# Performance work log

Measured on AMD Instinct MI355X. Metric: run time of the kernel, lower is better.

Reference implementation:

```python
import jax, jax.numpy as jnp
import numpy as np

NEG = -9999.0      # chart init / clip floor (np.clip a_min=-9999.0)
THRESH = -9000.0   # 'pseudo_score > -9000' acceptance gate
ARC_BONUS = 5.0    # '+ 5' added to every arc candidate


def _fill_chart(vinfo):
    """Eisner DP chart fill, faithful to the sequential numpy triple loop.
    vinfo: [N, N] arc scores. Returns (score_chart [N,N,2,2], backtrace [N,N,2,2]).
    Chart axes: [i, j, direction, completeness] as in the torch source.
    Parallelized over span start i and split q; sequential over width k via scan.
    Sequential-update subtleties of the original q-loop are reproduced exactly:
      * complete (0,1) at q=i reads the (0,0) cell as it stands after only the
        q=i incomplete update ('part00');
      * complete (1,1) at q=j reads the fully updated (1,0) cell ('new10');
      * complete (0,1) at q=j and (1,1) at q=i are strict-improvement no-ops;
      * ties keep the earliest q (jnp.argmax returns first occurrence).
    """
    N = vinfo.shape[0]
    idx = jnp.arange(N)
    ii = idx[:, None]   # span start i
    mm = idx[None, :]   # split offset m; q = i + m
    S = jnp.full((N, N, 2, 2), NEG, dtype=vinfo.dtype).at[idx, idx].set(0.0)
    BT = jnp.zeros((N, N, 2, 2), dtype=jnp.int32)

    def step(carry, k):
        S, BT = carry
        j = idx + k
        row_ok = j < N
        okb = row_ok[:, None]
        jc = jnp.minimum(j, N - 1)
        jb = jc[:, None]
        q = ii + mm
        qc = jnp.minimum(q, N - 1)
        q1c = jnp.minimum(q + 1, N - 1)

        # ---- incomplete spans (0,0) and (1,0): q in [i, j-1]  <=>  m in [0, k-1]
        base = jnp.where((mm < k) & okb,
                         S[:, :, 1, 1][ii, qc] + S[:, :, 0, 1][q1c, jb],
                         -jnp.inf)                      # [N (i), N (m)]
        vL = vinfo[jc, idx][:, None]   # vinfo[j, i] -> arc j<-...: head j
        vR = vinfo[idx, jc][:, None]   # vinfo[i, j]
        p00 = jnp.maximum(base + vL + ARC_BONUS, NEG)
        p10 = jnp.maximum(base + vR + ARC_BONUS, NEG)
        m00 = jnp.max(p00, axis=1); q00 = idx + jnp.argmax(p00, axis=1)
        m10 = jnp.max(p10, axis=1); q10 = idx + jnp.argmax(p10, axis=1)
        ok00 = row_ok & (m00 > THRESH)
        ok10 = row_ok & (m10 > THRESH)
        # chart[i,j,0,0] as it stands right after the q=i iteration
        part00 = jnp.where(row_ok & (p00[:, 0] > THRESH), p00[:, 0], NEG)
        new10 = jnp.where(ok10, m10, NEG)

        m_mid = (mm >= 1) & (mm < k) & okb
        # ---- complete (0,1): q=i uses partially built (0,0); q=j is a no-op
        c01 = jnp.where(m_mid, S[:, :, 0, 1][ii, qc] + S[:, :, 0, 0][qc, jb], -jnp.inf)
        c01 = c01.at[:, 0].set(jnp.where(row_ok, part00, -jnp.inf))
        p01 = jnp.maximum(c01, NEG)
        m01 = jnp.max(p01, axis=1); q01 = idx + jnp.argmax(p01, axis=1)
        ok01 = row_ok & (m01 > THRESH)

        # ---- complete (1,1): q=i is a no-op; q=j uses freshly updated (1,0)
        c11 = jnp.where(m_mid, S[:, :, 1, 0][ii, qc] + S[:, :, 1, 1][qc, jb], -jnp.inf)
        c11 = jnp.where((mm == k) & okb, new10[:, None], c11)
        p11 = jnp.maximum(c11, NEG)
        m11 = jnp.max(p11, axis=1); q11 = idx + jnp.argmax(p11, axis=1)
        ok11 = row_ok & (m11 > THRESH)

        def upd(S, BT, a, b, ok, val, qarg):
            S = S.at[idx, jc, a, b].set(jnp.where(ok, val, S[idx, jc, a, b]))
            BT = BT.at[idx, jc, a, b].set(
                jnp.where(ok, qarg, BT[idx, jc, a, b]).astype(jnp.int32))
            return S, BT

        S, BT = upd(S, BT, 0, 0, ok00, m00, q00)
        S, BT = upd(S, BT, 1, 0, ok10, m10, q10)
        S, BT = upd(S, BT, 0, 1, ok01, m01, q01)
        S, BT = upd(S, BT, 1, 1, ok11, m11, q11)
        return (S, BT), None

    (S, BT), _ = jax.lax.scan(step, (S, BT), jnp.arange(1, N))
    return S, BT


def setup_inputs() -> dict:
    key = jax.random.key(0)
    B, N = 64, 128
    b_vinfo_mtx = jax.random.normal(key, (B, N, N), dtype=jnp.float32)
    b_buffer_size = jnp.full((B,), N, dtype=jnp.int32)
    return {"b_vinfo_mtx": b_vinfo_mtx, "b_buffer_size": b_buffer_size}


def reference(b_vinfo_mtx, b_buffer_size):
    # All sentences use the full buffer (b_buffer_size == N), so the batch is
    # processed as one vmapped chart fill.
    scores, backtrace = jax.vmap(_fill_chart)(b_vinfo_mtx)
    return scores, backtrace
```

## Files before the change

### kernel.cpp

```cpp
#include <hip/hip_runtime.h>
#include <stdint.h>

static constexpr int kN = 128;
static constexpr int kTri = (kN * (kN - 1)) / 2;
static constexpr int kTriD = (kN * (kN + 1)) / 2;
static constexpr int kThreads = 1024;
static constexpr float kNeg = -9999.0f;
static constexpr float kThresh = -9000.0f;
static constexpr float kArcBonus = 5.0f;
static constexpr int kDynLds = kTriD * 16;
static constexpr int kCMax = 9;

__device__ __forceinline__ int rowBase(int i) { return (i * (2 * kN - 1 - i)) / 2; }
__device__ __forceinline__ int colBaseD(int c) { return (c * (c + 1)) / 2; }

__device__ __forceinline__ void ldsBarrier() {
    asm volatile("s_waitcnt lgkmcnt(0)\n\ts_barrier" ::: "memory");
}

template <int CTRL>
__device__ __forceinline__ float dppMax(float x) {
    const int y = __builtin_amdgcn_update_dpp(__float_as_int(x), __float_as_int(x),
                                              CTRL, 0xF, 0xF, true);
    return fmaxf(x, __int_as_float(y));
}
template <int CTRL>
__device__ __forceinline__ int dppMinI(int x) {
    const int y = __builtin_amdgcn_update_dpp(x, x, CTRL, 0xF, 0xF, true);
    return (y < x) ? y : x;
}

__device__ __forceinline__ int lpOf(int k) {
    if (k <= 16) return 0;
    if (k < 64) return 3;
    return 4;
}
__device__ __forceinline__ void mapStatic(int nk, int tid, int& i, int& j, bool& act) {
    const int lp = lpOf(nk);
    i = tid >> lp;
    j = i + nk;
    act = i < (kN - nk);
}

__device__ __forceinline__ float4 writeCell(float4* __restrict__ Q4,
                                            uint32_t* __restrict__ wsBT,
                                            int i, int j, int k,
                                            float gb, int ib, float vLc, float vRc,
                                            float v01, int i01, float v11, int i11) {
    const float v00 = (gb + vLc) + kArcBonus;
    const float v10 = (gb + vRc) + kArcBonus;
    const float new10 = (v10 > kThresh) ? v10 : kNeg;
    if (new10 > v11) { v11 = new10; i11 = k; }
    float4 w = make_float4(kNeg, kNeg, kNeg, kNeg);
    uint32_t p = 0;
    if (v00 > kThresh) { w.x = v00; p |= (uint32_t)(i + ib); }
    if (v01 > kThresh) { w.z = v01; p |= (uint32_t)(i + i01) << 8; }
    if (v10 > kThresh) { w.w = v10; p |= (uint32_t)(i + ib) << 16; }
    if (v11 > kThresh) { w.y = v11; p |= (uint32_t)(i + i11) << 24; }
    Q4[colBaseD(j) + i] = w;
    wsBT[rowBase(i) + k - 1] = p;
    return w;
}

__device__ __forceinline__ void doStepSerialReg(int k, int tid,
                                                float4* __restrict__ Q4,
                                                uint32_t* __restrict__ wsBT,
                                                const float* __restrict__ v,
                                                int& ci, int& cj, bool& cact,
                                                float& vL, float& vR,
                                                float (&sr11)[17], float (&sr01)[17],
                                                float (&sr10)[17]) {
    const int i = ci, j = cj;
    const bool act = cact;
    const float vLc = vL, vRc = vR;
    float bmax = -3.0e38f, v01 = -3.0e38f, v11 = -3.0e38f;
    int ib = 0, i01 = 0, i11 = 0x7FFFFFFF;
    if (act) {
        const int qjb = colBaseD(j);
        float4 cur = Q4[qjb + i + 1];
        bmax = cur.z; ib = 0;
        const float p00 = (cur.z + vLc) + kArcBonus;
        v01 = (p00 > kThresh) ? p00 : kNeg; i01 = 0;
#pragma unroll
        for (int m = 1; m < 16; ++m) {
            if (m < k) {
                const float4 nxt = Q4[qjb + i + m + 1];
                const float base = sr11[m] + nxt.z;
                const float p01v = sr01[m] + cur.x;
                const float p11v = sr10[m] + cur.y;
                if (base > bmax) { bmax = base; ib = m; }
                if (p01v > v01) { v01 = p01v; i01 = m; }
                if (p11v > v11) { v11 = p11v; i11 = m; }
                cur = nxt;
            }
        }
    }
    if (k + 1 < kN) {
        mapStatic(k + 1, tid, ci, cj, cact);
        vL = cact ? v[cj * kN + ci] : 0.f;
        vR = cact ? v[ci * kN + cj] : 0.f;
    }
    if (act) {
        const float4 w = writeCell(Q4, wsBT, i, j, k, bmax, ib, vLc, vRc,
                                   v01, i01, v11, i11);
        sr11[k] = w.y; sr01[k] = w.z; sr10[k] = w.w;
    }
}

template <int LP, int C>
__device__ __forceinline__ void preloadRow(int k0, int tid,
                                           const float4* __restrict__ Q4,
                                           float (&r11)[kCMax], float (&r01)[kCMax],
                                           float (&r10)[kCMax]) {
    constexpr int P = 1 << LP;
    const int i = tid >> LP;
    const int l = tid & (P - 1);
    const int mlo = l * C;
    const int mstart = mlo ? mlo : 1;
    const bool act = i < (kN - k0);
#pragma unroll
    for (int c = 0; c < C; ++c) {
        const int m = mstart + c;
        if (act && (m < mlo + C) && (m <= k0 - 1)) {
            const float4 d = Q4[colBaseD(i + m) + i];
            r11[c] = d.y; r01[c] = d.z; r10[c] = d.w;
        }
    }
}

template <int LP, int C>
__device__ __forceinline__ void fwInit(int k0, int tid,
                                       const float (&r11)[kCMax], const float (&r01)[kCMax],
                                       const float (&r10)[kCMax],
                                       float& fw11, float& fw01, float& fw10) {
    constexpr int P = 1 << LP;
    const int l = tid & (P - 1);
    const int mlo = l * C;
    const int mstart = mlo ? mlo : 1;
#pragma unroll
    for (int c = 0; c < C; ++c) {
        if (mstart + c == k0 - 1) { fw11 = r11[c]; fw01 = r01[c]; fw10 = r10[c]; }
    }
}

template <int LP, int C>
__device__ __forceinline__ void doStepC(int k, int tid,
                                        float4* __restrict__ Q4,
                                        uint32_t* __restrict__ wsBT,
                                        const float* __restrict__ v,
                                        int& ci, int& cj, bool& cact,
                                        float& vL, float& vR,
                                        float (&r11)[kCMax], float (&r01)[kCMax],
                                        float (&r10)[kCMax],
                                        float& fw11, float& fw01, float& fw10) {
    constexpr int P = 1 << LP;
    static_assert(P <= 16, "reductions must stay pure-DPP");
    const int i = ci, j = cj;
    const bool act = cact;
    const float vLc = vL, vRc = vR;
    const int l = tid & (P - 1);
    const int mlo = l * C;
    const int mstart = mlo ? mlo : 1;
    const int mhi = (mlo + C < k) ? (mlo + C) : k;
    const bool waveActive = (((tid & ~63) >> LP) < (kN - k));

    float bmax = -3.0e38f, v01 = -3.0e38f, v11 = -3.0e38f;
    int ib = 0x7FFFFFFF, i01 = 0x7FFFFFFF, i11 = 0x7FFFFFFF;

    const int mf = k - 1;
    const bool lact = waveActive && act && (mstart < mhi);
    const int qjb = colBaseD(j);
    float4 cur = make_float4(0.f, 0.f, 0.f, 0.f);
    if (lact) cur = Q4[qjb + i + mstart];
    if (act && mlo == 0) {
        bmax = cur.z; ib = 0;
        const float p00 = (cur.z + vLc) + kArcBonus;
        v01 = (p00 > kThresh) ? p00 : kNeg; i01 = 0;
    }
#pragma unroll
    for (int c = 0; c < C; ++c) {
        const int m = mstart + c;
        const bool isF = (m == mf);
        const float a11 = isF ? fw11 : r11[c];
        const float a01 = isF ? fw01 : r01[c];
        const float a10 = isF ? fw10 : r10[c];
        r11[c] = a11; r01[c] = a01; r10[c] = a10;
        const bool on = lact && (m < mhi);
        if (on) {
            const float4 nxt = Q4[qjb + i + m + 1];
            const float base = a11 + nxt.z;
            const float p01v = a01 + cur.x;
            const float p11v = a10 + cur.y;
            if (base > bmax) { bmax = base; ib = m; }
            if (p01v > v01) { v01 = p01v; i01 = m; }
            if (p11v > v11) { v11 = p11v; i11 = m; }
            cur = nxt;
        }
    }

    if (k + 1 < kN) {
        mapStatic(k + 1, tid, ci, cj, cact);
        vL = cact ? v[cj * kN + ci] : 0.f;
        vR = cact ? v[ci * kN + cj] : 0.f;
    }

    if (waveActive) {
        float gB = dppMax<0x141>(dppMax<0x4E>(dppMax<0xB1>(bmax)));
        float g01 = dppMax<0x141>(dppMax<0x4E>(dppMax<0xB1>(v01)));
        float g11 = dppMax<0x141>(dppMax<0x4E>(dppMax<0xB1>(v11)));
        if constexpr (P == 16) {
            gB = dppMax<0x140>(gB); g01 = dppMax<0x140>(g01); g11 = dppMax<0x140>(g11);
        }
        int cB = (bmax == gB) ? ib : 0x7FFFFFFF;
        int c01 = (v01 == g01) ? i01 : 0x7FFFFFFF;
        int c11 = (v11 == g11) ? i11 : 0x7FFFFFFF;
        cB = dppMinI<0x141>(dppMinI<0x4E>(dppMinI<0xB1>(cB)));
        c01 = dppMinI<0x141>(dppMinI<0x4E>(dppMinI<0xB1>(c01)));
        c11 = dppMinI<0x141>(dppMinI<0x4E>(dppMinI<0xB1>(c11)));
        if constexpr (P == 16) {
            cB = dppMinI<0x140>(cB); c01 = dppMinI<0x140>(c01); c11 = dppMinI<0x140>(c11);
        }

        const float v10f = (gB + vRc) + kArcBonus;
        const float new10 = (v10f > kThresh) ? v10f : kNeg;
        float v11m = g11;
        if (new10 > v11m) v11m = new10;
        fw11 = (v11m > kThresh) ? v11m : kNeg;
        fw01 = (g01 > kThresh) ? g01 : kNeg;
        fw10 = (v10f > kThresh) ? v10f : kNeg;

        if (act && l == 0) {
            writeCell(Q4, wsBT, i, j, k, gB, cB, vLc, vRc, g01, c01, g11, c11);
        }
    }
}

__global__ __launch_bounds__(kThreads) void eisner_dp(
    const float* __restrict__ vinfo,
    float* __restrict__ outS,
    float* __restrict__ outBT,
    uint32_t* __restrict__ btPacked)
{
    extern __shared__ float4 Q4[];

    const int tid = threadIdx.x;
    const int b = blockIdx.x;
    const float* v = vinfo + (size_t)b * kN * kN;
    uint32_t* wsBT = btPacked + (size_t)b * kTri;

    const float4 zeroq = make_float4(0.f, 0.f, 0.f, 0.f);
    if (tid < kN) Q4[colBaseD(tid) + tid] = zeroq;

    int ci, cj; bool cact;
    mapStatic(1, tid, ci, cj, cact);
    float vL = cact ? v[cj * kN + ci] : 0.f;
    float vR = cact ? v[ci * kN + cj] : 0.f;
    __syncthreads();

    {
        float sr11[17], sr01[17], sr10[17];
#pragma unroll
        for (int k = 1; k <= 16; ++k) {
            doStepSerialReg(k, tid, Q4, wsBT, v, ci, cj, cact, vL, vR,
                            sr11, sr01, sr10);
            ldsBarrier();
        }
    }

    float r11[kCMax], r01[kCMax], r10[kCMax];
    float fw11 = kNeg, fw01 = kNeg, fw10 = kNeg;
#pragma unroll
    for (int c = 0; c < kCMax; ++c) { r11[c] = kNeg; r01[c] = kNeg; r10[c] = kNeg; }

    preloadRow<3, 5>(17, tid, Q4, r11, r01, r10);
    fwInit<3, 5>(17, tid, r11, r01, r10, fw11, fw01, fw10);
    for (int k = 17; k < 40; ++k) {
        doStepC<3, 5>(k, tid, Q4, wsBT, v, ci, cj, cact, vL, vR,
                      r11, r01, r10, fw11, fw01, fw10);
        ldsBarrier();
    }
    preloadRow<3, 9>(40, tid, Q4, r11, r01, r10);
    fwInit<3, 9>(40, tid, r11, r01, r10, fw11, fw01, fw10);
    for (int k = 40; k < 64; ++k) {
        doStepC<3, 9>(k, tid, Q4, wsBT, v, ci, cj, cact, vL, vR,
                      r11, r01, r10, fw11, fw01, fw10);
        ldsBarrier();
    }
    preloadRow<4, 7>(64, tid, Q4, r11, r01, r10);
    fwInit<4, 7>(64, tid, r11, r01, r10, fw11, fw01, fw10);
    for (int k = 64; k < 112; ++k) {
        doStepC<4, 7>(k, tid, Q4, wsBT, v, ci, cj, cact, vL, vR,
                      r11, r01, r10, fw11, fw01, fw10);
        ldsBarrier();
    }
    preloadRow<4, 9>(112, tid, Q4, r11, r01, r10);
    fwInit<4, 9>(112, tid, r11, r01, r10, fw11, fw01, fw10);
    for (int k = 112; k < 128; ++k) {
        doStepC<4, 9>(k, tid, Q4, wsBT, v, ci, cj, cact, vL, vR,
                      r11, r01, r10, fw11, fw01, fw10);
        ldsBarrier();
    }

    __syncthreads();

    float4* gS4 = (float4*)(outS + (size_t)b * kN * kN * 4);
    float4* gB4 = (float4*)(outBT + (size_t)b * kN * kN * 4);
    const float4 negq = make_float4(kNeg, kNeg, kNeg, kNeg);
    for (int c = tid; c < kN * kN; c += kThreads) {
        const int i = c >> 7, j = c & (kN - 1);
        if (i < j) {
            const float4 q = Q4[colBaseD(j) + i];
            gS4[c] = make_float4(q.x, q.z, q.w, q.y);
            const uint32_t p = wsBT[rowBase(i) + (j - i - 1)];
            gB4[c] = make_float4((float)(p & 255u), (float)((p >> 8) & 255u),
                                 (float)((p >> 16) & 255u), (float)(p >> 24));
        } else if (i == j) {
            gS4[c] = zeroq;
            gB4[c] = zeroq;
        } else {
            gS4[c] = negq;
            gB4[c] = zeroq;
        }
    }
}

extern "C" void kernel_launch(void* const* d_in, const int* in_sizes, int n_in,
                              void* d_out, int out_size, void* d_ws, size_t ws_size,
                              hipStream_t stream) {
    (void)n_in; (void)out_size; (void)ws_size;
    const float* vinfo = (const float*)d_in[0];
    const int B = in_sizes[1];
    float* outS = (float*)d_out;
    float* outBT = outS + (size_t)B * kN * kN * 4;
    uint32_t* btPacked = (uint32_t*)d_ws;

    hipFuncSetAttribute(reinterpret_cast<const void*>(eisner_dp),
                        hipFuncAttributeMaxDynamicSharedMemorySize, kDynLds);

    eisner_dp<<<dim3(B), dim3(kThreads), kDynLds, stream>>>(vinfo, outS, outBT, btPacked);
}
```

Measured before the change: 236.4 us.

## Replace per-step block barriers with per-wave LDS flag point-to-point sync

Drops the workgroup-wide barrier after every DP width step. Each wave now spin-waits on an LDS flag published by its neighbouring wave, reflecting the one-sided dependency between span rows. Waves whose spans run out finish early and publish a sentinel, so the others are not held back by idle waves. The risks are spin-polling overhead, LDS memory-ordering issues with volatile flags, and deadlock if a dependency assumption is wrong.

```diff
diff --git a/kernel.cpp b/kernel.cpp
--- a/kernel.cpp
+++ b/kernel.cpp
@@ -8,15 +8,12 @@
 static constexpr float kNeg = -9999.0f;
 static constexpr float kThresh = -9000.0f;
 static constexpr float kArcBonus = 5.0f;
-static constexpr int kDynLds = kTriD * 16;
+static constexpr int kFlagInts = 5 * 17;
+static constexpr int kDynLds = kTriD * 16 + kFlagInts * 4;
 static constexpr int kCMax = 9;
 
 __device__ __forceinline__ int rowBase(int i) { return (i * (2 * kN - 1 - i)) / 2; }
 __device__ __forceinline__ int colBaseD(int c) { return (c * (c + 1)) / 2; }
-
-__device__ __forceinline__ void ldsBarrier() {
-    asm volatile("s_waitcnt lgkmcnt(0)\n\ts_barrier" ::: "memory");
-}
 
 template <int CTRL>
 __device__ __forceinline__ float dppMax(float x) {
@@ -28,6 +25,15 @@
 __device__ __forceinline__ int dppMinI(int x) {
     const int y = __builtin_amdgcn_update_dpp(x, x, CTRL, 0xF, 0xF, true);
     return (y < x) ? y : x;
+}
+
+__device__ __forceinline__ void spinWait(volatile const int* f, int need) {
+    while (*f < need) __builtin_amdgcn_s_sleep(2);
+    asm volatile("" ::: "memory");
+}
+__device__ __forceinline__ void publish(volatile int* f, int val, int laneId) {
+    asm volatile("s_waitcnt lgkmcnt(0)" ::: "memory");
+    if (laneId == 0) *f = val;
 }
 
 __device__ __forceinline__ int lpOf(int k) {
@@ -235,6 +241,48 @@
     }
 }
 
+__device__ __forceinline__ void runPhaseSerial(int tid, int laneId, int w,
+        float4* __restrict__ Q4, volatile int* flg,
+        uint32_t* __restrict__ wsBT, const float* __restrict__ v) {
+    if ((w << 6) >= kN - 1) return;
+    int ci, cj; bool cact;
+    mapStatic(1, tid, ci, cj, cact);
+    float vL = cact ? v[cj * kN + ci] : 0.f;
+    float vR = cact ? v[ci * kN + cj] : 0.f;
+    float sr11[17], sr01[17], sr10[17];
+#pragma unroll
+    for (int k = 1; k <= 16; ++k) {
+        spinWait(flg + (w + 1), k - 1);
+        doStepSerialReg(k, tid, Q4, wsBT, v, ci, cj, cact, vL, vR, sr11, sr01, sr10);
+        publish(flg + w, k, laneId);
+    }
+}
+
+template <int LP, int C>
+__device__ __forceinline__ void runPhaseC(int k0, int k1, int tid, int laneId, int w,
+        float4* __restrict__ Q4, volatile int* flg,
+        uint32_t* __restrict__ wsBT, const float* __restrict__ v,
+        float (&r11)[kCMax], float (&r01)[kCMax], float (&r10)[kCMax]) {
+    const int firstGroup = (w << 6) >> LP;
+    if (firstGroup >= kN - k0) return;
+    int ci, cj; bool cact;
+    mapStatic(k0, tid, ci, cj, cact);
+    float vL = cact ? v[cj * kN + ci] : 0.f;
+    float vR = cact ? v[ci * kN + cj] : 0.f;
+    float fw11 = kNeg, fw01 = kNeg, fw10 = kNeg;
+    preloadRow<LP, C>(k0, tid, Q4, r11, r01, r10);
+    fwInit<LP, C>(k0, tid, r11, r01, r10, fw11, fw01, fw10);
+    const int kD = kN - firstGroup;
+    const int kEnd = (k1 < kD) ? k1 : kD;
+    for (int k = k0; k < kEnd; ++k) {
+        spinWait(flg + (w + 1), k - 1);
+        doStepC<LP, C>(k, tid, Q4, wsBT, v, ci, cj, cact, vL, vR,
+                       r11, r01, r10, fw11, fw01, fw10);
+        publish(flg + w, k, laneId);
+    }
+    if (kD < k1) publish(flg + w, 127, laneId);
+}
+
 __global__ __launch_bounds__(kThreads) void eisner_dp(
     const float* __restrict__ vinfo,
     float* __restrict__ outS,
@@ -242,8 +290,11 @@
     uint32_t* __restrict__ btPacked)
 {
     extern __shared__ float4 Q4[];
+    int* flagBase = (int*)(Q4 + kTriD);
 
     const int tid = threadIdx.x;
+    const int laneId = tid & 63;
+    const int w = tid >> 6;
     const int b = blockIdx.x;
     const float* v = vinfo + (size_t)b * kN * kN;
     uint32_t* wsBT = btPacked + (size_t)b * kTri;
@@ -251,55 +302,36 @@
     const float4 zeroq = make_float4(0.f, 0.f, 0.f, 0.f);
     if (tid < kN) Q4[colBaseD(tid) + tid] = zeroq;
 
-    int ci, cj; bool cact;
-    mapStatic(1, tid, ci, cj, cact);
-    float vL = cact ? v[cj * kN + ci] : 0.f;
-    float vR = cact ? v[ci * kN + cj] : 0.f;
-    __syncthreads();
-
-    {
-        float sr11[17], sr01[17], sr10[17];
-#pragma unroll
-        for (int k = 1; k <= 16; ++k) {
-            doStepSerialReg(k, tid, Q4, wsBT, v, ci, cj, cact, vL, vR,
-                            sr11, sr01, sr10);
-            ldsBarrier();
-        }
-    }
+    if (tid < kFlagInts) {
+        const int p = tid / 17, s = tid - p * 17;
+        int k0v = 1, lp = 0;
+        if (p == 1)      { k0v = 17;  lp = 3; }
+        else if (p == 2) { k0v = 40;  lp = 3; }
+        else if (p == 3) { k0v = 64;  lp = 4; }
+        else if (p == 4) { k0v = 112; lp = 4; }
+        int val = 127;
+        if (s < 16) {
+            const int fg = (s << 6) >> lp;
+            if (fg < kN - k0v) val = k0v - 1;
+        }
+        flagBase[tid] = val;
+    }
+    __syncthreads();
+
+    runPhaseSerial(tid, laneId, w, Q4, flagBase + 0, wsBT, v);
+    __syncthreads();
 
     float r11[kCMax], r01[kCMax], r10[kCMax];
-    float fw11 = kNeg, fw01 = kNeg, fw10 = kNeg;
 #pragma unroll
     for (int c = 0; c < kCMax; ++c) { r11[c] = kNeg; r01[c] = kNeg; r10[c] = kNeg; }
 
-    preloadRow<3, 5>(17, tid, Q4, r11, r01, r10);
-    fwInit<3, 5>(17, tid, r11, r01, r10, fw11, fw01, fw10);
-    for (int k = 17; k < 40; ++k) {
-        doStepC<3, 5>(k, tid, Q4, wsBT, v, ci, cj, cact, vL, vR,
-                      r11, r01, r10, fw11, fw01, fw10);
-        ldsBarrier();
-    }
-    preloadRow<3, 9>(40, tid, Q4, r11, r01, r10);
-    fwInit<3, 9>(40, tid, r11, r01, r10, fw11, fw01, fw10);
-    for (int k = 40; k < 64; ++k) {
-        doStepC<3, 9>(k, tid, Q4, wsBT, v, ci, cj, cact, vL, vR,
-                      r11, r01, r10, fw11, fw01, fw10);
-        ldsBarrier();
-    }
-    preloadRow<4, 7>(64, tid, Q4, r11, r01, r10);
-    fwInit<4, 7>(64, tid, r11, r01, r10, fw11, fw01, fw10);
-    for (int k = 64; k < 112; ++k) {
-        doStepC<4, 7>(k, tid, Q4, wsBT, v, ci, cj, cact, vL, vR,
-                      r11, r01, r10, fw11, fw01, fw10);
-        ldsBarrier();
-    }
-    preloadRow<4, 9>(112, tid, Q4, r11, r01, r10);
-    fwInit<4, 9>(112, tid, r11, r01, r10, fw11, fw01, fw10);
-    for (int k = 112; k < 128; ++k) {
-        doStepC<4, 9>(k, tid, Q4, wsBT, v, ci, cj, cact, vL, vR,
-                      r11, r01, r10, fw11, fw01, fw10);
-        ldsBarrier();
-    }
+    runPhaseC<3, 5>(17, 40, tid, laneId, w, Q4, flagBase + 17, wsBT, v, r11, r01, r10);
+    __syncthreads();
+    runPhaseC<3, 9>(40, 64, tid, laneId, w, Q4, flagBase + 34, wsBT, v, r11, r01, r10);
+    __syncthreads();
+    runPhaseC<4, 7>(64, 112, tid, laneId, w, Q4, flagBase + 51, wsBT, v, r11, r01, r10);
+    __syncthreads();
+    runPhaseC<4, 9>(112, 128, tid, laneId, w, Q4, flagBase + 68, wsBT, v, r11, r01, r10);
 
     __syncthreads();
 
```

Measured after the change: 253.1 us. 7.1% more time.
